# Kernel tuning notes

Measured on AMD Instinct MI355X. Metric: run time of the kernel, lower is better.

## Reference

```python
import jax, jax.numpy as jnp
import numpy as np

T, B, C, H, W = 6, 8, 192, 112, 112
K = 3          # max_typhoon_number
H0, W0 = 56, 56


def setup_inputs() -> dict:
    key = jax.random.key(0)
    k1, k2, k3, k4, k5 = jax.random.split(key, 5)
    x = jax.random.normal(k1, (T, B, C, H, W), dtype=jnp.float32)
    gcn_masks = jax.random.randint(k2, (B, T, K, H0, W0), 0, 2).astype(jnp.int32)
    W_emb = jax.random.normal(k3, (C, C), dtype=jnp.float32) * (1.0 / np.sqrt(C))
    W_gcn = jax.random.normal(k4, (C, C), dtype=jnp.float32) * (1.0 / np.sqrt(C))
    b_gcn = jax.random.normal(k5, (C,), dtype=jnp.float32) * (1.0 / np.sqrt(C))
    return {"x": x, "gcn_masks": gcn_masks, "W_emb": W_emb, "W_gcn": W_gcn, "b_gcn": b_gcn}


def reference(x, gcn_masks, W_emb, W_gcn, b_gcn):
    # x: [T,B,C,H,W]; gcn_masks: [B,T,K,H0,W0] binary
    Tn, Bn, Cn, Hn, Wn = x.shape
    Kn = gcn_masks.shape[2]
    # F.interpolate(mode='nearest') to (H,W)
    m = jax.image.resize(gcn_masks.astype(jnp.float32), (Bn, Tn, Kn, Hn, Wn), method='nearest')
    # masked adaptive avg-pool (mean over ALL HxW pixels, as AdaptiveAvgPool2d(1))
    # node features per (b, t, k): [B,T,K,C]
    feat = jnp.einsum('tbchw,btkhw->btkc', x, m) / (Hn * Wn)
    node = feat.reshape(Bn, Tn * Kn, Cn)             # [B, N, C], N = T*K = 18
    # dynamic adjacency: softmax over last dim of node @ node^T
    adj = jax.nn.softmax(jnp.einsum('bnc,bmc->bnm', node, node), axis=-1)
    # embedding layer (nn.Linear no bias): node @ W_emb^T
    aaa = jnp.einsum('bnc,dc->bnd', node, W_emb)
    # GCN: adj @ (aaa @ W_gcn) + b_gcn
    support = jnp.einsum('bnd,de->bne', aaa, W_gcn)
    out = jnp.einsum('bnm,bme->bne', adj, support) + b_gcn   # [B, N, C]
    # nearest 'upsample' of 1x1 -> HxW is a broadcast; scatter-combine over K
    outk = out.reshape(Bn, Tn, Kn, Cn)
    residual = jnp.einsum('btkc,btkhw->tbchw', outk, m)
    return x + residual
```

## Files before the change

kernel.cpp:

```cpp
#include <hip/hip_runtime.h>

#define T_ 6
#define B_ 8
#define C_ 192
#define H_ 112
#define W_ 112
#define K_ 3
#define H0_ 56
#define W0_ 56
#define N_ (T_ * K_)
#define HW_ (H_ * W_)
#define HW0_ (H0_ * W0_)

__global__ __launch_bounds__(256) void build_code_kernel(
    const int* __restrict__ masks, unsigned char* __restrict__ code) {
  int idx = blockIdx.x * 256 + threadIdx.x;
  if (idx >= B_ * T_ * HW0_) return;
  int p = idx % HW0_;
  int bt = idx / HW0_;
  const int base = bt * K_ * HW0_;
  int c0 = masks[base + 0 * HW0_ + p];
  int c1 = masks[base + 1 * HW0_ + p];
  int c2 = masks[base + 2 * HW0_ + p];
  code[idx] = (unsigned char)((c0 & 1) | ((c1 & 1) << 1) | ((c2 & 1) << 2));
}

__global__ __launch_bounds__(256) void pool_kernel(
    const float* __restrict__ x, const unsigned char* __restrict__ code,
    float* __restrict__ feat) {
  int blk = blockIdx.x;
  int c = blk % C_;
  int tb = blk / C_;
  int b = tb % B_;
  int t = tb / B_;

  const float4* xp = (const float4*)(x + (size_t)blk * HW_);
  const unsigned char* cp = code + (b * T_ + t) * HW0_;

  float s0 = 0.f, s1 = 0.f, s2 = 0.f;
  for (int i = threadIdx.x; i < HW_ / 4; i += 256) {
    float4 v = xp[i];
    int p = i * 4;
    int h = p / W_;
    int w = p - h * W_;
    const unsigned char* crow = cp + (h >> 1) * W0_ + (w >> 1);
    int ca = crow[0];
    int cb = crow[1];
    float pa = v.x + v.y;
    float pb = v.z + v.w;
    s0 += (ca & 1 ? pa : 0.f) + (cb & 1 ? pb : 0.f);
    s1 += (ca & 2 ? pa : 0.f) + (cb & 2 ? pb : 0.f);
    s2 += (ca & 4 ? pa : 0.f) + (cb & 4 ? pb : 0.f);
  }

  for (int off = 32; off > 0; off >>= 1) {
    s0 += __shfl_down(s0, off);
    s1 += __shfl_down(s1, off);
    s2 += __shfl_down(s2, off);
  }
  __shared__ float red[4][3];
  int lane = threadIdx.x & 63;
  int wid = threadIdx.x >> 6;
  if (lane == 0) {
    red[wid][0] = s0;
    red[wid][1] = s1;
    red[wid][2] = s2;
  }
  __syncthreads();
  if (threadIdx.x == 0) {
    float f0 = red[0][0] + red[1][0] + red[2][0] + red[3][0];
    float f1 = red[0][1] + red[1][1] + red[2][1] + red[3][1];
    float f2 = red[0][2] + red[1][2] + red[2][2] + red[3][2];
    float* fb = feat + ((b * T_ + t) * K_) * C_ + c;
    fb[0 * C_] = f0;
    fb[1 * C_] = f1;
    fb[2 * C_] = f2;
  }
}

__global__ __launch_bounds__(256) void gcn_kernel(
    const float* __restrict__ feat, const float* __restrict__ W_emb,
    const float* __restrict__ W_gcn, const float* __restrict__ b_gcn,
    float* __restrict__ outk) {
  int b = blockIdx.x;
  int tid = threadIdx.x;
  __shared__ float node[N_][C_];
  __shared__ float aaa[N_][C_];
  __shared__ float sup[N_][C_];
  __shared__ float adj[N_][N_];

  const float inv_hw = 1.0f / (float)HW_;
  for (int i = tid; i < N_ * C_; i += 256)
    node[i / C_][i % C_] = feat[b * N_ * C_ + i] * inv_hw;
  __syncthreads();

  for (int i = tid; i < N_ * N_; i += 256) {
    int n = i / N_, m = i % N_;
    float s = 0.f;
    for (int c = 0; c < C_; ++c) s += node[n][c] * node[m][c];
    adj[n][m] = s;
  }
  __syncthreads();

  if (tid < N_) {
    float mx = -1e30f;
    for (int m = 0; m < N_; ++m) mx = fmaxf(mx, adj[tid][m]);
    float tmp[N_];
    float sum = 0.f;
    for (int m = 0; m < N_; ++m) {
      tmp[m] = __expf(adj[tid][m] - mx);
      sum += tmp[m];
    }
    float inv = 1.0f / sum;
    for (int m = 0; m < N_; ++m) adj[tid][m] = tmp[m] * inv;
  }
  __syncthreads();

  for (int i = tid; i < N_ * C_; i += 256) {
    int n = i / C_, d = i % C_;
    const float* we = W_emb + d * C_;
    float s = 0.f;
    for (int c = 0; c < C_; ++c) s += node[n][c] * we[c];
    aaa[n][d] = s;
  }
  __syncthreads();

  for (int i = tid; i < N_ * C_; i += 256) {
    int n = i / C_, e = i % C_;
    float s = 0.f;
    for (int d = 0; d < C_; ++d) s += aaa[n][d] * W_gcn[d * C_ + e];
    sup[n][e] = s;
  }
  __syncthreads();

  for (int i = tid; i < N_ * C_; i += 256) {
    int n = i / C_, e = i % C_;
    float s = b_gcn[e];
    for (int m = 0; m < N_; ++m) s += adj[n][m] * sup[m][e];
    outk[b * N_ * C_ + i] = s;
  }
}

__global__ __launch_bounds__(256) void out_kernel(
    const float* __restrict__ x, const unsigned char* __restrict__ code,
    const float* __restrict__ outk, float* __restrict__ out) {
  int blk = blockIdx.x;
  int c = blk % C_;
  int tb = blk / C_;
  int b = tb % B_;
  int t = tb / B_;

  const float* ob = outk + ((b * T_ + t) * K_) * C_ + c;
  float o0 = ob[0 * C_], o1 = ob[1 * C_], o2 = ob[2 * C_];

  const float4* xp = (const float4*)(x + (size_t)blk * HW_);
  float4* op = (float4*)(out + (size_t)blk * HW_);
  const unsigned char* cp = code + (b * T_ + t) * HW0_;

  for (int i = threadIdx.x; i < HW_ / 4; i += 256) {
    float4 v = xp[i];
    int p = i * 4;
    int h = p / W_;
    int w = p - h * W_;
    const unsigned char* crow = cp + (h >> 1) * W0_ + (w >> 1);
    int ca = crow[0];
    int cb = crow[1];
    float addA = (ca & 1 ? o0 : 0.f) + (ca & 2 ? o1 : 0.f) + (ca & 4 ? o2 : 0.f);
    float addB = (cb & 1 ? o0 : 0.f) + (cb & 2 ? o1 : 0.f) + (cb & 4 ? o2 : 0.f);
    v.x += addA;
    v.y += addA;
    v.z += addB;
    v.w += addB;
    op[i] = v;
  }
}

extern "C" void kernel_launch(void* const* d_in, const int* in_sizes, int n_in,
                              void* d_out, int out_size, void* d_ws,
                              size_t ws_size, hipStream_t stream) {
  const float* x = (const float*)d_in[0];
  const int* masks = (const int*)d_in[1];
  const float* W_emb = (const float*)d_in[2];
  const float* W_gcn = (const float*)d_in[3];
  const float* b_gcn = (const float*)d_in[4];
  float* out = (float*)d_out;

  unsigned char* code = (unsigned char*)d_ws;
  float* feat = (float*)((char*)d_ws + 150528);
  float* outk = (float*)((char*)d_ws + 150528 + 110592);

  {
    int n = B_ * T_ * HW0_;
    build_code_kernel<<<(n + 255) / 256, 256, 0, stream>>>(masks, code);
  }
  pool_kernel<<<T_ * B_ * C_, 256, 0, stream>>>(x, code, feat);
  gcn_kernel<<<B_, 256, 0, stream>>>(feat, W_emb, W_gcn, b_gcn, outk);
  out_kernel<<<T_ * B_ * C_, 256, 0, stream>>>(x, code, outk, out);
}
```

Measured before the change: 977.2 us.

## Precompute fused W_emb^T·W_gcn weight, reverse out_kernel block order for cache reuse

Fuses the two chained linear layers into one precomputed CxC matrix Wf = W_emb^T @ W_gcn, computed in a combined prep kernel alongside the mask code build, so the 8-block GCN kernel does one GEMM instead of two. The 1/HW scale moves into the pool kernel, node shared memory is padded, and small loops are unrolled. out_kernel now walks blocks in reverse order so it starts on the x slices pool_kernel touched last, which may still sit in the large cache. The extra Wf computation is redundant work per call, done by 192 extra blocks.

```diff
diff --git a/kernel.cpp b/kernel.cpp
--- a/kernel.cpp
+++ b/kernel.cpp
@@ -11,18 +11,32 @@
 #define N_ (T_ * K_)
 #define HW_ (H_ * W_)
 #define HW0_ (H0_ * W0_)
-
-__global__ __launch_bounds__(256) void build_code_kernel(
-    const int* __restrict__ masks, unsigned char* __restrict__ code) {
-  int idx = blockIdx.x * 256 + threadIdx.x;
-  if (idx >= B_ * T_ * HW0_) return;
-  int p = idx % HW0_;
-  int bt = idx / HW0_;
-  const int base = bt * K_ * HW0_;
-  int c0 = masks[base + 0 * HW0_ + p];
-  int c1 = masks[base + 1 * HW0_ + p];
-  int c2 = masks[base + 2 * HW0_ + p];
-  code[idx] = (unsigned char)((c0 & 1) | ((c1 & 1) << 1) | ((c2 & 1) << 2));
+#define CODE_BLOCKS 588
+
+__global__ __launch_bounds__(256) void prep_kernel(
+    const int* __restrict__ masks, unsigned char* __restrict__ code,
+    const float* __restrict__ W_emb, const float* __restrict__ W_gcn,
+    float* __restrict__ Wf) {
+  int blk = blockIdx.x;
+  if (blk < CODE_BLOCKS) {
+    int idx = blk * 256 + threadIdx.x;
+    int p = idx % HW0_;
+    int bt = idx / HW0_;
+    const int base = bt * K_ * HW0_;
+    int c0 = masks[base + 0 * HW0_ + p];
+    int c1 = masks[base + 1 * HW0_ + p];
+    int c2 = masks[base + 2 * HW0_ + p];
+    code[idx] = (unsigned char)((c0 & 1) | ((c1 & 1) << 1) | ((c2 & 1) << 2));
+  } else {
+    int c = blk - CODE_BLOCKS;
+    int e = threadIdx.x;
+    if (e < C_) {
+      float s = 0.f;
+#pragma unroll 4
+      for (int d = 0; d < C_; ++d) s += W_emb[d * C_ + c] * W_gcn[d * C_ + e];
+      Wf[c * C_ + e] = s;
+    }
+  }
 }
 
 __global__ __launch_bounds__(256) void pool_kernel(
@@ -68,9 +82,10 @@
   }
   __syncthreads();
   if (threadIdx.x == 0) {
-    float f0 = red[0][0] + red[1][0] + red[2][0] + red[3][0];
-    float f1 = red[0][1] + red[1][1] + red[2][1] + red[3][1];
-    float f2 = red[0][2] + red[1][2] + red[2][2] + red[3][2];
+    const float inv_hw = 1.0f / (float)HW_;
+    float f0 = (red[0][0] + red[1][0] + red[2][0] + red[3][0]) * inv_hw;
+    float f1 = (red[0][1] + red[1][1] + red[2][1] + red[3][1]) * inv_hw;
+    float f2 = (red[0][2] + red[1][2] + red[2][2] + red[3][2]) * inv_hw;
     float* fb = feat + ((b * T_ + t) * K_) * C_ + c;
     fb[0 * C_] = f0;
     fb[1 * C_] = f1;
@@ -79,24 +94,22 @@
 }
 
 __global__ __launch_bounds__(256) void gcn_kernel(
-    const float* __restrict__ feat, const float* __restrict__ W_emb,
-    const float* __restrict__ W_gcn, const float* __restrict__ b_gcn,
-    float* __restrict__ outk) {
+    const float* __restrict__ feat, const float* __restrict__ Wf,
+    const float* __restrict__ b_gcn, float* __restrict__ outk) {
   int b = blockIdx.x;
   int tid = threadIdx.x;
-  __shared__ float node[N_][C_];
-  __shared__ float aaa[N_][C_];
+  __shared__ float node[N_][C_ + 1];
   __shared__ float sup[N_][C_];
   __shared__ float adj[N_][N_];
 
-  const float inv_hw = 1.0f / (float)HW_;
   for (int i = tid; i < N_ * C_; i += 256)
-    node[i / C_][i % C_] = feat[b * N_ * C_ + i] * inv_hw;
+    node[i / C_][i % C_] = feat[b * N_ * C_ + i];
   __syncthreads();
 
   for (int i = tid; i < N_ * N_; i += 256) {
     int n = i / N_, m = i % N_;
     float s = 0.f;
+#pragma unroll 8
     for (int c = 0; c < C_; ++c) s += node[n][c] * node[m][c];
     adj[n][m] = s;
   }
@@ -104,31 +117,26 @@
 
   if (tid < N_) {
     float mx = -1e30f;
+#pragma unroll
     for (int m = 0; m < N_; ++m) mx = fmaxf(mx, adj[tid][m]);
     float tmp[N_];
     float sum = 0.f;
+#pragma unroll
     for (int m = 0; m < N_; ++m) {
       tmp[m] = __expf(adj[tid][m] - mx);
       sum += tmp[m];
     }
     float inv = 1.0f / sum;
+#pragma unroll
     for (int m = 0; m < N_; ++m) adj[tid][m] = tmp[m] * inv;
-  }
-  __syncthreads();
-
-  for (int i = tid; i < N_ * C_; i += 256) {
-    int n = i / C_, d = i % C_;
-    const float* we = W_emb + d * C_;
-    float s = 0.f;
-    for (int c = 0; c < C_; ++c) s += node[n][c] * we[c];
-    aaa[n][d] = s;
   }
   __syncthreads();
 
   for (int i = tid; i < N_ * C_; i += 256) {
     int n = i / C_, e = i % C_;
     float s = 0.f;
-    for (int d = 0; d < C_; ++d) s += aaa[n][d] * W_gcn[d * C_ + e];
+#pragma unroll 4
+    for (int c = 0; c < C_; ++c) s += node[n][c] * Wf[c * C_ + e];
     sup[n][e] = s;
   }
   __syncthreads();
@@ -136,6 +144,7 @@
   for (int i = tid; i < N_ * C_; i += 256) {
     int n = i / C_, e = i % C_;
     float s = b_gcn[e];
+#pragma unroll
     for (int m = 0; m < N_; ++m) s += adj[n][m] * sup[m][e];
     outk[b * N_ * C_ + i] = s;
   }
@@ -144,7 +153,7 @@
 __global__ __launch_bounds__(256) void out_kernel(
     const float* __restrict__ x, const unsigned char* __restrict__ code,
     const float* __restrict__ outk, float* __restrict__ out) {
-  int blk = blockIdx.x;
+  int blk = (T_ * B_ * C_ - 1) - blockIdx.x;
   int c = blk % C_;
   int tb = blk / C_;
   int b = tb % B_;
@@ -188,12 +197,11 @@
   unsigned char* code = (unsigned char*)d_ws;
   float* feat = (float*)((char*)d_ws + 150528);
   float* outk = (float*)((char*)d_ws + 150528 + 110592);
-
-  {
-    int n = B_ * T_ * HW0_;
-    build_code_kernel<<<(n + 255) / 256, 256, 0, stream>>>(masks, code);
-  }
+  float* Wf = (float*)((char*)d_ws + 150528 + 110592 + 110592);
+
+  prep_kernel<<<CODE_BLOCKS + C_, 256, 0, stream>>>(masks, code, W_emb, W_gcn,
+                                                    Wf);
   pool_kernel<<<T_ * B_ * C_, 256, 0, stream>>>(x, code, feat);
-  gcn_kernel<<<B_, 256, 0, stream>>>(feat, W_emb, W_gcn, b_gcn, outk);
+  gcn_kernel<<<B_, 256, 0, stream>>>(feat, Wf, b_gcn, outk);
   out_kernel<<<T_ * B_ * C_, 256, 0, stream>>>(x, code, outk, out);
 }
```

Result: no change. 968.1 us (-0.9%).
